# Performance work log

Measured on AMD Instinct MI355X. Metric: run time of the kernel, lower is better.

Reference implementation:

```python
import jax, jax.numpy as jnp
import numpy as np

N_NODES = 50000
N_EDGES = 500000
D_MODEL = 256
N_HEADS = 8
D_K = D_MODEL // N_HEADS


def setup_inputs() -> dict:
    key = jax.random.key(0)
    ks = jax.random.split(key, 12)
    s = 1.0 / np.sqrt(D_MODEL)
    inp = {
        "query": jax.random.normal(ks[0], (N_NODES, D_MODEL), dtype=jnp.float32),
        "key": jax.random.normal(ks[1], (N_NODES, D_MODEL), dtype=jnp.float32),
        "value": jax.random.normal(ks[2], (N_NODES, D_MODEL), dtype=jnp.float32),
        "edges": jax.random.randint(ks[3], (2, N_EDGES), 0, N_NODES, dtype=jnp.int64),
        # four nn.Linear(d_model, d_model) layers: q, k, v, out
        "Wq": jax.random.uniform(ks[4], (D_MODEL, D_MODEL), jnp.float32, -s, s),
        "bq": jax.random.uniform(ks[5], (D_MODEL,), jnp.float32, -s, s),
        "Wk": jax.random.uniform(ks[6], (D_MODEL, D_MODEL), jnp.float32, -s, s),
        "bk": jax.random.uniform(ks[7], (D_MODEL,), jnp.float32, -s, s),
        "Wv": jax.random.uniform(ks[8], (D_MODEL, D_MODEL), jnp.float32, -s, s),
        "bv": jax.random.uniform(ks[9], (D_MODEL,), jnp.float32, -s, s),
        "Wo": jax.random.uniform(ks[10], (D_MODEL, D_MODEL), jnp.float32, -s, s),
        "bo": jax.random.uniform(ks[11], (D_MODEL,), jnp.float32, -s, s),
    }
    return inp


def reference(query, key, value, edges, Wq, bq, Wk, bk, Wv, bv, Wo, bo):
    N = query.shape[0]
    # linear projections (torch Linear: x @ W.T + b), view as [N, h, d_k]
    q = (query @ Wq.T + bq).reshape(N, N_HEADS, D_K)
    k = (key @ Wk.T + bk).reshape(N, N_HEADS, D_K)
    v = (value @ Wv.T + bv).reshape(N, N_HEADS, D_K)

    dst, src = edges[0], edges[1]
    # per-edge dot-product scores [E, h]
    scores = jnp.einsum("ehd,ehd->eh", q[dst], k[src]) / jnp.sqrt(
        jnp.asarray(D_K, dtype=q.dtype)
    )
    # segment softmax over destination node neighborhoods (per head)
    m = jax.ops.segment_max(scores, dst, num_segments=N)  # [N, h]
    ex = jnp.exp(scores - m[dst])
    den = jax.ops.segment_sum(ex, dst, num_segments=N)  # [N, h]
    p_attn = ex / den[dst]  # [E, h]

    # weighted scatter-sum of gathered values -> [N, h, d_k]
    out = jax.ops.segment_sum(p_attn[:, :, None] * v[src], dst, num_segments=N)
    out = out.reshape(N, D_MODEL)
    return out @ Wo.T + bo
```

## Files before the change

### kernel.cpp

```cpp
#include <hip/hip_runtime.h>
#include <hip/hip_bf16.h>
#include <cstdint>

#define D_MODEL 256
#define NHEADS 8
#define DK 32
#define LDSPAD 8
#define LDSROW (D_MODEL + LDSPAD)
#define LDSROWF (D_MODEL + 4)

typedef float f32x4 __attribute__((ext_vector_type(4)));
typedef __bf16 bf16x8 __attribute__((ext_vector_type(8)));

__device__ __forceinline__ unsigned short f2bf_rne(float f) {
    unsigned int u = __float_as_uint(f);
    u += 0x7FFF + ((u >> 16) & 1);
    return (unsigned short)(u >> 16);
}
__device__ __forceinline__ float bf2f(unsigned short h) {
    return __uint_as_float(((unsigned int)h) << 16);
}

__global__ void conv_weights(const float* __restrict__ W0, const float* __restrict__ W1,
                             const float* __restrict__ W2, const float* __restrict__ W3,
                             unsigned short* __restrict__ out) {
    int i = blockIdx.x * blockDim.x + threadIdx.x;
    if (i >= 4 * 8192) return;
    const int w    = i >> 13;
    const int rem  = i & 8191;
    const int lane = rem & 63;
    const int kk   = (rem >> 6) & 7;
    const int ntile= rem >> 9;
    const int row  = ntile * 16 + (lane & 15);
    const int col  = kk * 32 + (lane >> 4) * 8;
    const float* Wsrc = (w == 0) ? W0 : (w == 1) ? W1 : (w == 2) ? W2 : W3;
    const float* sp = Wsrc + (size_t)row * D_MODEL + col;
    float4 x0 = *(const float4*)sp;
    float4 x1 = *(const float4*)(sp + 4);
    unsigned short* dp = out + (size_t)w * D_MODEL * D_MODEL + (size_t)rem * 8;
    ushort4 o0, o1;
    o0.x = f2bf_rne(x0.x); o0.y = f2bf_rne(x0.y); o0.z = f2bf_rne(x0.z); o0.w = f2bf_rne(x0.w);
    o1.x = f2bf_rne(x1.x); o1.y = f2bf_rne(x1.y); o1.z = f2bf_rne(x1.z); o1.w = f2bf_rne(x1.w);
    *(ushort4*)dp = o0;
    *(ushort4*)(dp + 4) = o1;
}

__global__ __launch_bounds__(256, 4) void gemm_qkv(
    const float* __restrict__ Aq, const float* __restrict__ Ak, const float* __restrict__ Av,
    const unsigned short* __restrict__ Wsw,
    const float* __restrict__ bq, const float* __restrict__ bk, const float* __restrict__ bv,
    unsigned short* __restrict__ qbuf, unsigned short* __restrict__ kvbuf, int M)
{
    __shared__ __align__(16) unsigned short smem[64 * LDSROW];

    const int which = blockIdx.y;
    const float* A = (which == 0) ? Aq : (which == 1) ? Ak : Av;
    const float* bias = (which == 0) ? bq : (which == 1) ? bk : bv;
    const unsigned short* Wb = Wsw + (size_t)which * D_MODEL * D_MODEL;
    unsigned short* outp = (which == 0) ? qbuf : kvbuf;
    const int out_stride = (which == 0) ? D_MODEL : 2 * D_MODEL;
    const int out_off    = (which == 2) ? D_MODEL : 0;

    const int lane  = threadIdx.x & 63;
    const int wave  = threadIdx.x >> 6;
    const int m0    = blockIdx.x * 64;
    const int mrow  = lane & 15;
    const int quad  = lane >> 4;

#pragma unroll
    for (int i = 0; i < 16; ++i) {
        const int g = i * 256 + threadIdx.x;
        const int r = g >> 6, c4 = g & 63;
        const int grow = min(m0 + r, M - 1);
        float4 x = *(const float4*)(A + (size_t)grow * D_MODEL + c4 * 4);
        ushort4 o;
        o.x = f2bf_rne(x.x); o.y = f2bf_rne(x.y);
        o.z = f2bf_rne(x.z); o.w = f2bf_rne(x.w);
        *(ushort4*)(smem + r * LDSROW + c4 * 4) = o;
    }
    __syncthreads();

    f32x4 acc[4][4] = {};

#pragma unroll
    for (int kk = 0; kk < 8; ++kk) {
        bf16x8 bfr[4];
#pragma unroll
        for (int ni = 0; ni < 4; ++ni) {
            const int ntile = wave * 4 + ni;
            bfr[ni] = *(const bf16x8*)(Wb + ((size_t)(ntile * 8 + kk) * 64 + lane) * 8);
        }
        bf16x8 afr[4];
#pragma unroll
        for (int mi = 0; mi < 4; ++mi)
            afr[mi] = *(const bf16x8*)(smem + (mi * 16 + mrow) * LDSROW + kk * 32 + quad * 8);
#pragma unroll
        for (int mi = 0; mi < 4; ++mi)
#pragma unroll
            for (int ni = 0; ni < 4; ++ni)
                acc[mi][ni] = __builtin_amdgcn_mfma_f32_16x16x32_bf16(
                    afr[mi], bfr[ni], acc[mi][ni], 0, 0, 0);
    }

    __syncthreads();
#pragma unroll
    for (int ni = 0; ni < 4; ++ni) {
        const int col = wave * 64 + ni * 16 + mrow;
        const float bv2 = bias[col];
#pragma unroll
        for (int mi = 0; mi < 4; ++mi)
#pragma unroll
            for (int r = 0; r < 4; ++r)
                smem[(mi * 16 + quad * 4 + r) * LDSROW + col] = f2bf_rne(acc[mi][ni][r] + bv2);
    }
    __syncthreads();
#pragma unroll
    for (int i = 0; i < 8; ++i) {
        const int g = i * 256 + threadIdx.x;
        const int r = g >> 5, c8 = g & 31;
        const int grow = m0 + r;
        if (grow < M) {
            bf16x8 x = *(const bf16x8*)(smem + r * LDSROW + c8 * 8);
            *(bf16x8*)(outp + (size_t)grow * out_stride + out_off + c8 * 8) = x;
        }
    }
}

__global__ __launch_bounds__(256, 4) void gemm_out(
    const unsigned short* __restrict__ Ab, const unsigned short* __restrict__ Wb,
    const float* __restrict__ bias, float* __restrict__ outp, int M)
{
    __shared__ __align__(16) char smem_raw[32 * LDSROWF * 4];
    unsigned short* smemA = (unsigned short*)smem_raw;
    float*          smemF = (float*)smem_raw;

    const int lane  = threadIdx.x & 63;
    const int wave  = threadIdx.x >> 6;
    const int m0    = blockIdx.x * 32;
    const int mrow  = lane & 15;
    const int quad  = lane >> 4;

#pragma unroll
    for (int i = 0; i < 4; ++i) {
        const int g = i * 256 + threadIdx.x;
        const int r = g >> 5, c8 = g & 31;
        const int grow = min(m0 + r, M - 1);
        bf16x8 x = *(const bf16x8*)(Ab + (size_t)grow * D_MODEL + c8 * 8);
        *(bf16x8*)(smemA + r * LDSROW + c8 * 8) = x;
    }
    __syncthreads();

    f32x4 acc[2][4] = {};

#pragma unroll
    for (int kk = 0; kk < 8; ++kk) {
        bf16x8 bfr[4];
#pragma unroll
        for (int ni = 0; ni < 4; ++ni) {
            const int ntile = wave * 4 + ni;
            bfr[ni] = *(const bf16x8*)(Wb + ((size_t)(ntile * 8 + kk) * 64 + lane) * 8);
        }
        bf16x8 afr[2];
#pragma unroll
        for (int mi = 0; mi < 2; ++mi)
            afr[mi] = *(const bf16x8*)(smemA + (mi * 16 + mrow) * LDSROW + kk * 32 + quad * 8);
#pragma unroll
        for (int mi = 0; mi < 2; ++mi)
#pragma unroll
            for (int ni = 0; ni < 4; ++ni)
                acc[mi][ni] = __builtin_amdgcn_mfma_f32_16x16x32_bf16(
                    afr[mi], bfr[ni], acc[mi][ni], 0, 0, 0);
    }

    __syncthreads();
#pragma unroll
    for (int ni = 0; ni < 4; ++ni) {
        const int col = wave * 64 + ni * 16 + mrow;
        const float bv2 = bias[col];
#pragma unroll
        for (int mi = 0; mi < 2; ++mi)
#pragma unroll
            for (int r = 0; r < 4; ++r)
                smemF[(mi * 16 + quad * 4 + r) * LDSROWF + col] = acc[mi][ni][r] + bv2;
    }
    __syncthreads();
#pragma unroll
    for (int i = 0; i < 8; ++i) {
        const int g = i * 256 + threadIdx.x;
        const int r = g >> 6, c4 = g & 63;
        const int grow = m0 + r;
        if (grow < M) {
            float4 x = *(const float4*)(smemF + r * LDSROWF + c4 * 4);
            *(float4*)(outp + (size_t)grow * D_MODEL + c4 * 4) = x;
        }
    }
}

__global__ void hist_kernel(const int* __restrict__ dst, int E, int* __restrict__ counts) {
    int i = blockIdx.x * blockDim.x + threadIdx.x;
    if (i < E) atomicAdd(&counts[dst[i]], 1);
}

__global__ void block_reduce_kernel(const int* __restrict__ counts, int N,
                                    int* __restrict__ blockSums) {
    const int g = blockIdx.x * 256 + threadIdx.x;
    int v = (g < N) ? counts[g] : 0;
#pragma unroll
    for (int d = 1; d < 64; d <<= 1) v += __shfl_xor(v, d);
    __shared__ int ws[4];
    if ((threadIdx.x & 63) == 0) ws[threadIdx.x >> 6] = v;
    __syncthreads();
    if (threadIdx.x == 0) blockSums[blockIdx.x] = ws[0] + ws[1] + ws[2] + ws[3];
}

__global__ void scan_blocks_kernel(int* __restrict__ blockSums, int G) {
    __shared__ int sh[256];
    const int t = threadIdx.x;
    int v = (t < G) ? blockSums[t] : 0;
    sh[t] = v;
    __syncthreads();
#pragma unroll
    for (int off = 1; off < 256; off <<= 1) {
        int add = (t >= off) ? sh[t - off] : 0;
        __syncthreads();
        sh[t] += add;
        __syncthreads();
    }
    if (t < G) blockSums[t] = sh[t] - v;
}

__global__ void scan_write_kernel(const int* __restrict__ counts, int N,
                                  const int* __restrict__ blockOffsets,
                                  int* __restrict__ offsets) {
    const int g = blockIdx.x * 256 + threadIdx.x;
    const int t = threadIdx.x;
    int v = (g < N) ? counts[g] : 0;
    __shared__ int sh[256];
    sh[t] = v;
    __syncthreads();
#pragma unroll
    for (int off = 1; off < 256; off <<= 1) {
        int add = (t >= off) ? sh[t - off] : 0;
        __syncthreads();
        sh[t] += add;
        __syncthreads();
    }
    if (g <= N) offsets[g] = sh[t] - v + blockOffsets[blockIdx.x];
}

__global__ void fill_kernel(const int* __restrict__ dst, const int* __restrict__ src, int E,
                            const int* __restrict__ offsets, int* __restrict__ cursor,
                            int* __restrict__ ssrc) {
    int i = blockIdx.x * blockDim.x + threadIdx.x;
    if (i < E) {
        int d = dst[i];
        int r = atomicAdd(&cursor[d], 1);
        ssrc[offsets[d] + r] = src[i];
    }
}

__global__ __launch_bounds__(256) void attn_kernel(
    const unsigned short* __restrict__ qb, const unsigned short* __restrict__ kv,
    const int* __restrict__ offsets, const int* __restrict__ ssrc,
    unsigned short* __restrict__ attn, int N)
{
    const int node = blockIdx.x * 4 + (threadIdx.x >> 6);
    if (node >= N) return;
    const int lane = threadIdx.x & 63;

    ushort4 qu = *(const ushort4*)(qb + (size_t)node * D_MODEL + 4 * lane);
    const float sc = 0.17677669529663689f;
    float qx = bf2f(qu.x) * sc, qy = bf2f(qu.y) * sc,
          qz = bf2f(qu.z) * sc, qw = bf2f(qu.w) * sc;

    float m = -INFINITY, l = 0.f;
    float ax = 0.f, ay = 0.f, az = 0.f, aw = 0.f;

    const int e0 = offsets[node], e1 = offsets[node + 1];
    int e = e0;

    for (; e + 3 < e1; e += 4) {
        int s0 = ssrc[e], s1 = ssrc[e + 1], s2 = ssrc[e + 2], s3 = ssrc[e + 3];
        const unsigned short* b0 = kv + (size_t)s0 * 512;
        const unsigned short* b1 = kv + (size_t)s1 * 512;
        const unsigned short* b2 = kv + (size_t)s2 * 512;
        const unsigned short* b3 = kv + (size_t)s3 * 512;
        ushort4 k0 = *(const ushort4*)(b0 + 4 * lane);
        ushort4 k1 = *(const ushort4*)(b1 + 4 * lane);
        ushort4 k2 = *(const ushort4*)(b2 + 4 * lane);
        ushort4 k3 = *(const ushort4*)(b3 + 4 * lane);
        ushort4 v0 = *(const ushort4*)(b0 + D_MODEL + 4 * lane);
        ushort4 v1 = *(const ushort4*)(b1 + D_MODEL + 4 * lane);
        ushort4 v2 = *(const ushort4*)(b2 + D_MODEL + 4 * lane);
        ushort4 v3 = *(const ushort4*)(b3 + D_MODEL + 4 * lane);

        float p0 = qx * bf2f(k0.x) + qy * bf2f(k0.y) + qz * bf2f(k0.z) + qw * bf2f(k0.w);
        float p1 = qx * bf2f(k1.x) + qy * bf2f(k1.y) + qz * bf2f(k1.z) + qw * bf2f(k1.w);
        float p2 = qx * bf2f(k2.x) + qy * bf2f(k2.y) + qz * bf2f(k2.z) + qw * bf2f(k2.w);
        float p3 = qx * bf2f(k3.x) + qy * bf2f(k3.y) + qz * bf2f(k3.z) + qw * bf2f(k3.w);
#pragma unroll
        for (int d = 1; d <= 4; d <<= 1) {
            p0 += __shfl_xor(p0, d);
            p1 += __shfl_xor(p1, d);
            p2 += __shfl_xor(p2, d);
            p3 += __shfl_xor(p3, d);
        }
        float mnew = fmaxf(fmaxf(fmaxf(m, p0), fmaxf(p1, p2)), p3);
        float alpha = __expf(m - mnew);
        float w0 = __expf(p0 - mnew), w1 = __expf(p1 - mnew);
        float w2 = __expf(p2 - mnew), w3 = __expf(p3 - mnew);
        ax = ax * alpha + w0 * bf2f(v0.x) + w1 * bf2f(v1.x) + w2 * bf2f(v2.x) + w3 * bf2f(v3.x);
        ay = ay * alpha + w0 * bf2f(v0.y) + w1 * bf2f(v1.y) + w2 * bf2f(v2.y) + w3 * bf2f(v3.y);
        az = az * alpha + w0 * bf2f(v0.z) + w1 * bf2f(v1.z) + w2 * bf2f(v2.z) + w3 * bf2f(v3.z);
        aw = aw * alpha + w0 * bf2f(v0.w) + w1 * bf2f(v1.w) + w2 * bf2f(v2.w) + w3 * bf2f(v3.w);
        l = l * alpha + w0 + w1 + w2 + w3;
        m = mnew;
    }
    for (; e < e1; ++e) {
        int s = ssrc[e];
        const unsigned short* b = kv + (size_t)s * 512;
        ushort4 ku = *(const ushort4*)(b + 4 * lane);
        ushort4 vu = *(const ushort4*)(b + D_MODEL + 4 * lane);
        float p = qx * bf2f(ku.x) + qy * bf2f(ku.y) + qz * bf2f(ku.z) + qw * bf2f(ku.w);
        p += __shfl_xor(p, 1);
        p += __shfl_xor(p, 2);
        p += __shfl_xor(p, 4);
        float mnew  = fmaxf(m, p);
        float alpha = __expf(m - mnew);
        float w     = __expf(p - mnew);
        ax = ax * alpha + w * bf2f(vu.x);
        ay = ay * alpha + w * bf2f(vu.y);
        az = az * alpha + w * bf2f(vu.z);
        aw = aw * alpha + w * bf2f(vu.w);
        l = l * alpha + w;
        m = mnew;
    }

    const float inv = (l > 0.f) ? 1.f / l : 0.f;
    ushort4 o;
    o.x = f2bf_rne(ax * inv);
    o.y = f2bf_rne(ay * inv);
    o.z = f2bf_rne(az * inv);
    o.w = f2bf_rne(aw * inv);
    *(ushort4*)(attn + (size_t)node * D_MODEL + 4 * lane) = o;
}

extern "C" void kernel_launch(void* const* d_in, const int* in_sizes, int n_in,
                              void* d_out, int out_size, void* d_ws, size_t ws_size,
                              hipStream_t stream)
{
    const float* query = (const float*)d_in[0];
    const float* key   = (const float*)d_in[1];
    const float* value = (const float*)d_in[2];
    const int*   edges = (const int*)d_in[3];
    const float* Wq = (const float*)d_in[4];
    const float* bq = (const float*)d_in[5];
    const float* Wk = (const float*)d_in[6];
    const float* bk = (const float*)d_in[7];
    const float* Wv = (const float*)d_in[8];
    const float* bv = (const float*)d_in[9];
    const float* Wo = (const float*)d_in[10];
    const float* bo = (const float*)d_in[11];
    float* out = (float*)d_out;

    const int N = in_sizes[0] / D_MODEL;
    const int E = in_sizes[3] / 2;
    const int* dst = edges;
    const int* src = edges + E;

    char* ws = (char*)d_ws;
    size_t off = 0;
    auto alloc = [&](size_t bytes) {
        void* p = ws + off;
        off += (bytes + 255) & ~(size_t)255;
        return p;
    };
    unsigned short* qbuf  = (unsigned short*)alloc((size_t)N * D_MODEL * 2);
    unsigned short* kvbuf = (unsigned short*)alloc((size_t)N * 2 * D_MODEL * 2);
    unsigned short* attnb = (unsigned short*)alloc((size_t)N * D_MODEL * 2);
    unsigned short* Wbuf  = (unsigned short*)alloc((size_t)4 * D_MODEL * D_MODEL * 2);
    int*            counts  = (int*)alloc((size_t)2 * N * 4);
    int*            offsets = (int*)alloc((size_t)(N + 1) * 4);
    int*            ssrc    = (int*)alloc((size_t)E * 4);
    int*            bsums   = (int*)alloc((size_t)256 * 4);

    hipMemsetAsync(counts, 0, (size_t)2 * N * 4, stream);

    conv_weights<<<(4 * 8192 + 255) / 256, 256, 0, stream>>>(Wq, Wk, Wv, Wo, Wbuf);

    const int mb64 = (N + 63) / 64;
    gemm_qkv<<<dim3(mb64, 3), 256, 0, stream>>>(query, key, value, Wbuf,
                                                bq, bk, bv, qbuf, kvbuf, N);

    const int eblocks = (E + 255) / 256;
    hist_kernel<<<eblocks, 256, 0, stream>>>(dst, E, counts);

    const int G = (N + 256) / 256;
    block_reduce_kernel<<<G, 256, 0, stream>>>(counts, N, bsums);
    scan_blocks_kernel<<<1, 256, 0, stream>>>(bsums, G);
    scan_write_kernel<<<G, 256, 0, stream>>>(counts, N, bsums, offsets);

    fill_kernel<<<eblocks, 256, 0, stream>>>(dst, src, E, offsets, counts + N, ssrc);
    attn_kernel<<<(N + 3) / 4, 256, 0, stream>>>(qbuf, kvbuf, offsets, ssrc, attnb, N);

    const int mb32 = (N + 31) / 32;
    gemm_out<<<mb32, 256, 0, stream>>>(attnb, Wbuf + 3 * D_MODEL * D_MODEL, bo, out, N);
}
```

Before: 374.8 us.

## Make projection GEMMs persistent with register-resident weight fragments

Both projection GEMM kernels become persistent grids of fixed size that loop over 32-row tiles. Each wave loads its whole weight slice and bias into registers once, instead of re-reading weight fragments from global memory for every tile. The QKV tile shrinks from 64 to 32 rows and launch bounds drop to 2 blocks per SIMD to fit the larger register footprint. The cost is lower occupancy, less latency hiding on the fp32 A loads, and an extra barrier per tile iteration.

```diff
diff --git a/kernel.cpp b/kernel.cpp
--- a/kernel.cpp
+++ b/kernel.cpp
@@ -8,6 +8,7 @@
 #define LDSPAD 8
 #define LDSROW (D_MODEL + LDSPAD)
 #define LDSROWF (D_MODEL + 4)
+#define PBLK 170
 
 typedef float f32x4 __attribute__((ext_vector_type(4)));
 typedef __bf16 bf16x8 __attribute__((ext_vector_type(8)));
@@ -45,13 +46,14 @@
     *(ushort4*)(dp + 4) = o1;
 }
 
-__global__ __launch_bounds__(256, 4) void gemm_qkv(
+__global__ __launch_bounds__(256, 2) void gemm_qkv(
     const float* __restrict__ Aq, const float* __restrict__ Ak, const float* __restrict__ Av,
     const unsigned short* __restrict__ Wsw,
     const float* __restrict__ bq, const float* __restrict__ bk, const float* __restrict__ bv,
-    unsigned short* __restrict__ qbuf, unsigned short* __restrict__ kvbuf, int M)
+    unsigned short* __restrict__ qbuf, unsigned short* __restrict__ kvbuf,
+    int M, int mtiles)
 {
-    __shared__ __align__(16) unsigned short smem[64 * LDSROW];
+    __shared__ __align__(16) unsigned short smem[32 * LDSROW];
 
     const int which = blockIdx.y;
     const float* A = (which == 0) ? Aq : (which == 1) ? Ak : Av;
@@ -63,72 +65,80 @@
 
     const int lane  = threadIdx.x & 63;
     const int wave  = threadIdx.x >> 6;
-    const int m0    = blockIdx.x * 64;
     const int mrow  = lane & 15;
     const int quad  = lane >> 4;
 
-#pragma unroll
-    for (int i = 0; i < 16; ++i) {
-        const int g = i * 256 + threadIdx.x;
-        const int r = g >> 6, c4 = g & 63;
-        const int grow = min(m0 + r, M - 1);
-        float4 x = *(const float4*)(A + (size_t)grow * D_MODEL + c4 * 4);
-        ushort4 o;
-        o.x = f2bf_rne(x.x); o.y = f2bf_rne(x.y);
-        o.z = f2bf_rne(x.z); o.w = f2bf_rne(x.w);
-        *(ushort4*)(smem + r * LDSROW + c4 * 4) = o;
-    }
-    __syncthreads();
-
-    f32x4 acc[4][4] = {};
-
-#pragma unroll
-    for (int kk = 0; kk < 8; ++kk) {
-        bf16x8 bfr[4];
+    bf16x8 bfr[4][8];
+#pragma unroll
+    for (int ni = 0; ni < 4; ++ni)
+#pragma unroll
+        for (int kk = 0; kk < 8; ++kk)
+            bfr[ni][kk] = *(const bf16x8*)(Wb + ((size_t)((wave * 4 + ni) * 8 + kk) * 64 + lane) * 8);
+
+    float bcol[4];
+#pragma unroll
+    for (int ni = 0; ni < 4; ++ni) bcol[ni] = bias[wave * 64 + ni * 16 + mrow];
+
+    for (int t = blockIdx.x; t < mtiles; t += PBLK) {
+        const int m0 = t * 32;
+
+#pragma unroll
+        for (int i = 0; i < 8; ++i) {
+            const int g = i * 256 + threadIdx.x;
+            const int r = g >> 6, c4 = g & 63;
+            const int grow = min(m0 + r, M - 1);
+            float4 x = *(const float4*)(A + (size_t)grow * D_MODEL + c4 * 4);
+            ushort4 o;
+            o.x = f2bf_rne(x.x); o.y = f2bf_rne(x.y);
+            o.z = f2bf_rne(x.z); o.w = f2bf_rne(x.w);
+            *(ushort4*)(smem + r * LDSROW + c4 * 4) = o;
+        }
+        __syncthreads();
+
+        f32x4 acc[2][4] = {};
+#pragma unroll
+        for (int kk = 0; kk < 8; ++kk) {
+            bf16x8 afr[2];
+#pragma unroll
+            for (int mi = 0; mi < 2; ++mi)
+                afr[mi] = *(const bf16x8*)(smem + (mi * 16 + mrow) * LDSROW + kk * 32 + quad * 8);
+#pragma unroll
+            for (int mi = 0; mi < 2; ++mi)
+#pragma unroll
+                for (int ni = 0; ni < 4; ++ni)
+                    acc[mi][ni] = __builtin_amdgcn_mfma_f32_16x16x32_bf16(
+                        afr[mi], bfr[ni][kk], acc[mi][ni], 0, 0, 0);
+        }
+
+        __syncthreads();
 #pragma unroll
         for (int ni = 0; ni < 4; ++ni) {
-            const int ntile = wave * 4 + ni;
-            bfr[ni] = *(const bf16x8*)(Wb + ((size_t)(ntile * 8 + kk) * 64 + lane) * 8);
-        }
-        bf16x8 afr[4];
-#pragma unroll
-        for (int mi = 0; mi < 4; ++mi)
-            afr[mi] = *(const bf16x8*)(smem + (mi * 16 + mrow) * LDSROW + kk * 32 + quad * 8);
-#pragma unroll
-        for (int mi = 0; mi < 4; ++mi)
-#pragma unroll
-            for (int ni = 0; ni < 4; ++ni)
-                acc[mi][ni] = __builtin_amdgcn_mfma_f32_16x16x32_bf16(
-                    afr[mi], bfr[ni], acc[mi][ni], 0, 0, 0);
-    }
-
-    __syncthreads();
-#pragma unroll
-    for (int ni = 0; ni < 4; ++ni) {
-        const int col = wave * 64 + ni * 16 + mrow;
-        const float bv2 = bias[col];
-#pragma unroll
-        for (int mi = 0; mi < 4; ++mi)
-#pragma unroll
-            for (int r = 0; r < 4; ++r)
-                smem[(mi * 16 + quad * 4 + r) * LDSROW + col] = f2bf_rne(acc[mi][ni][r] + bv2);
-    }
-    __syncthreads();
-#pragma unroll
-    for (int i = 0; i < 8; ++i) {
-        const int g = i * 256 + threadIdx.x;
-        const int r = g >> 5, c8 = g & 31;
-        const int grow = m0 + r;
-        if (grow < M) {
-            bf16x8 x = *(const bf16x8*)(smem + r * LDSROW + c8 * 8);
-            *(bf16x8*)(outp + (size_t)grow * out_stride + out_off + c8 * 8) = x;
-        }
-    }
-}
-
-__global__ __launch_bounds__(256, 4) void gemm_out(
+            const int col = wave * 64 + ni * 16 + mrow;
+#pragma unroll
+            for (int mi = 0; mi < 2; ++mi)
+#pragma unroll
+                for (int r = 0; r < 4; ++r)
+                    smem[(mi * 16 + quad * 4 + r) * LDSROW + col] =
+                        f2bf_rne(acc[mi][ni][r] + bcol[ni]);
+        }
+        __syncthreads();
+#pragma unroll
+        for (int i = 0; i < 4; ++i) {
+            const int g = i * 256 + threadIdx.x;
+            const int r = g >> 5, c8 = g & 31;
+            const int grow = m0 + r;
+            if (grow < M) {
+                bf16x8 x = *(const bf16x8*)(smem + r * LDSROW + c8 * 8);
+                *(bf16x8*)(outp + (size_t)grow * out_stride + out_off + c8 * 8) = x;
+            }
+        }
+        __syncthreads();
+    }
+}
+
+__global__ __launch_bounds__(256, 2) void gemm_out(
     const unsigned short* __restrict__ Ab, const unsigned short* __restrict__ Wb,
-    const float* __restrict__ bias, float* __restrict__ outp, int M)
+    const float* __restrict__ bias, float* __restrict__ outp, int M, int mtiles)
 {
     __shared__ __align__(16) char smem_raw[32 * LDSROWF * 4];
     unsigned short* smemA = (unsigned short*)smem_raw;
@@ -136,63 +146,70 @@
 
     const int lane  = threadIdx.x & 63;
     const int wave  = threadIdx.x >> 6;
-    const int m0    = blockIdx.x * 32;
     const int mrow  = lane & 15;
     const int quad  = lane >> 4;
 
-#pragma unroll
-    for (int i = 0; i < 4; ++i) {
-        const int g = i * 256 + threadIdx.x;
-        const int r = g >> 5, c8 = g & 31;
-        const int grow = min(m0 + r, M - 1);
-        bf16x8 x = *(const bf16x8*)(Ab + (size_t)grow * D_MODEL + c8 * 8);
-        *(bf16x8*)(smemA + r * LDSROW + c8 * 8) = x;
-    }
-    __syncthreads();
-
-    f32x4 acc[2][4] = {};
-
-#pragma unroll
-    for (int kk = 0; kk < 8; ++kk) {
-        bf16x8 bfr[4];
+    bf16x8 bfr[4][8];
+#pragma unroll
+    for (int ni = 0; ni < 4; ++ni)
+#pragma unroll
+        for (int kk = 0; kk < 8; ++kk)
+            bfr[ni][kk] = *(const bf16x8*)(Wb + ((size_t)((wave * 4 + ni) * 8 + kk) * 64 + lane) * 8);
+
+    float bcol[4];
+#pragma unroll
+    for (int ni = 0; ni < 4; ++ni) bcol[ni] = bias[wave * 64 + ni * 16 + mrow];
+
+    for (int t = blockIdx.x; t < mtiles; t += 3 * PBLK) {
+        const int m0 = t * 32;
+
+#pragma unroll
+        for (int i = 0; i < 4; ++i) {
+            const int g = i * 256 + threadIdx.x;
+            const int r = g >> 5, c8 = g & 31;
+            const int grow = min(m0 + r, M - 1);
+            bf16x8 x = *(const bf16x8*)(Ab + (size_t)grow * D_MODEL + c8 * 8);
+            *(bf16x8*)(smemA + r * LDSROW + c8 * 8) = x;
+        }
+        __syncthreads();
+
+        f32x4 acc[2][4] = {};
+#pragma unroll
+        for (int kk = 0; kk < 8; ++kk) {
+            bf16x8 afr[2];
+#pragma unroll
+            for (int mi = 0; mi < 2; ++mi)
+                afr[mi] = *(const bf16x8*)(smemA + (mi * 16 + mrow) * LDSROW + kk * 32 + quad * 8);
+#pragma unroll
+            for (int mi = 0; mi < 2; ++mi)
+#pragma unroll
+                for (int ni = 0; ni < 4; ++ni)
+                    acc[mi][ni] = __builtin_amdgcn_mfma_f32_16x16x32_bf16(
+                        afr[mi], bfr[ni][kk], acc[mi][ni], 0, 0, 0);
+        }
+
+        __syncthreads();
 #pragma unroll
         for (int ni = 0; ni < 4; ++ni) {
-            const int ntile = wave * 4 + ni;
-            bfr[ni] = *(const bf16x8*)(Wb + ((size_t)(ntile * 8 + kk) * 64 + lane) * 8);
-        }
-        bf16x8 afr[2];
-#pragma unroll
-        for (int mi = 0; mi < 2; ++mi)
-            afr[mi] = *(const bf16x8*)(smemA + (mi * 16 + mrow) * LDSROW + kk * 32 + quad * 8);
-#pragma unroll
-        for (int mi = 0; mi < 2; ++mi)
-#pragma unroll
-            for (int ni = 0; ni < 4; ++ni)
-                acc[mi][ni] = __builtin_amdgcn_mfma_f32_16x16x32_bf16(
-                    afr[mi], bfr[ni], acc[mi][ni], 0, 0, 0);
-    }
-
-    __syncthreads();
-#pragma unroll
-    for (int ni = 0; ni < 4; ++ni) {
-        const int col = wave * 64 + ni * 16 + mrow;
-        const float bv2 = bias[col];
-#pragma unroll
-        for (int mi = 0; mi < 2; ++mi)
-#pragma unroll
-            for (int r = 0; r < 4; ++r)
-                smemF[(mi * 16 + quad * 4 + r) * LDSROWF + col] = acc[mi][ni][r] + bv2;
-    }
-    __syncthreads();
-#pragma unroll
-    for (int i = 0; i < 8; ++i) {
-        const int g = i * 256 + threadIdx.x;
-        const int r = g >> 6, c4 = g & 63;
-        const int grow = m0 + r;
-        if (grow < M) {
-            float4 x = *(const float4*)(smemF + r * LDSROWF + c4 * 4);
-            *(float4*)(outp + (size_t)grow * D_MODEL + c4 * 4) = x;
-        }
+            const int col = wave * 64 + ni * 16 + mrow;
+#pragma unroll
+            for (int mi = 0; mi < 2; ++mi)
+#pragma unroll
+                for (int r = 0; r < 4; ++r)
+                    smemF[(mi * 16 + quad * 4 + r) * LDSROWF + col] = acc[mi][ni][r] + bcol[ni];
+        }
+        __syncthreads();
+#pragma unroll
+        for (int i = 0; i < 8; ++i) {
+            const int g = i * 256 + threadIdx.x;
+            const int r = g >> 6, c4 = g & 63;
+            const int grow = m0 + r;
+            if (grow < M) {
+                float4 x = *(const float4*)(smemF + r * LDSROWF + c4 * 4);
+                *(float4*)(outp + (size_t)grow * D_MODEL + c4 * 4) = x;
+            }
+        }
+        __syncthreads();
     }
 }
 
@@ -388,9 +405,9 @@
 
     conv_weights<<<(4 * 8192 + 255) / 256, 256, 0, stream>>>(Wq, Wk, Wv, Wo, Wbuf);
 
-    const int mb64 = (N + 63) / 64;
-    gemm_qkv<<<dim3(mb64, 3), 256, 0, stream>>>(query, key, value, Wbuf,
-                                                bq, bk, bv, qbuf, kvbuf, N);
+    const int mtiles = (N + 31) / 32;
+    gemm_qkv<<<dim3(PBLK, 3), 256, 0, stream>>>(query, key, value, Wbuf,
+                                                bq, bk, bv, qbuf, kvbuf, N, mtiles);
 
     const int eblocks = (E + 255) / 256;
     hist_kernel<<<eblocks, 256, 0, stream>>>(dst, E, counts);
@@ -403,6 +420,5 @@
     fill_kernel<<<eblocks, 256, 0, stream>>>(dst, src, E, offsets, counts + N, ssrc);
     attn_kernel<<<(N + 3) / 4, 256, 0, stream>>>(qbuf, kvbuf, offsets, ssrc, attnb, N);
 
-    const int mb32 = (N + 31) / 32;
-    gemm_out<<<mb32, 256, 0, stream>>>(attnb, Wbuf + 3 * D_MODEL * D_MODEL, bo, out, N);
-}
+    gemm_out<<<3 * PBLK, 256, 0, stream>>>(attnb, Wbuf + 3 * D_MODEL * D_MODEL, bo, out, N, mtiles);
+}
```

After: 358.0 us. 4.5% less time.
